# Kernel optimization log

Measured on AMD Instinct MI355X. Metric: run time of the kernel, lower is better.

The kernel has to match this reference:

```python
import jax, jax.numpy as jnp
import numpy as np

B, N, I, K = 2, 8192, 3, 10
LEN_IN = 3 * (K + 1) + 3 * K + I  # 69


def setup_inputs() -> dict:
    key = jax.random.key(0)
    ks = jax.random.split(key, 9)
    return {
        "position": jax.random.normal(ks[0], (B, N, 3), dtype=jnp.float32),
        "velocity": jax.random.normal(ks[1], (B, N, 3), dtype=jnp.float32),
        "init_config": jax.random.normal(ks[2], (B, I), dtype=jnp.float32),
        "W1": jax.random.normal(ks[3], (LEN_IN, 32), dtype=jnp.float32) * 0.1,
        "b1": jnp.zeros((32,), dtype=jnp.float32),
        "W2": jax.random.normal(ks[4], (32, 16), dtype=jnp.float32) * 0.1,
        "b2": jnp.zeros((16,), dtype=jnp.float32),
        "W3": jax.random.normal(ks[5], (16, 6), dtype=jnp.float32) * 0.1,
        "b3": jnp.zeros((6,), dtype=jnp.float32),
    }


def reference(position, velocity, init_config, W1, b1, W2, b2, W3, b3):
    b, n, _ = position.shape
    k = K
    # Squared Euclidean distances (same k-NN ordering as torch.cdist).
    sq = jnp.sum(position * position, axis=-1)  # [B,N]
    d2 = sq[:, :, None] + sq[:, None, :] - 2.0 * jnp.einsum(
        "bnd,bmd->bnm", position, position
    )  # [B,N,N]
    # k+1 nearest (self included), sorted ascending by distance.
    _, idx = jax.lax.top_k(-d2, k + 1)  # [B,N,k+1]
    # Gather neighbor velocities (incl. self) and positions (excl. self).
    vel_nn = jnp.take_along_axis(
        velocity[:, None, :, :], idx[..., None], axis=2
    )  # [B,N,k+1,3]
    pos_nn = jnp.take_along_axis(
        position[:, None, :, :], idx[:, :, 1:, None], axis=2
    )  # [B,N,k,3]
    offset = pos_nn - position[:, :, None, :]  # [B,N,k,3]
    feats = jnp.concatenate(
        [
            vel_nn.reshape(b, n, 3 * (k + 1)),
            offset.reshape(b, n, 3 * k),
            jnp.broadcast_to(init_config[:, None, :], (b, n, init_config.shape[-1])),
        ],
        axis=-1,
    )  # [B,N,6k+3+I]
    h = feats @ W1 + b1
    h = h @ W2 + b2
    pred = h @ W3 + b3  # [B,N,6]
    pred = jnp.concatenate([pred[..., :3] + position, pred[..., 3:]], axis=-1)
    return pred
```

## Files before the change

### kernel.cpp

```cpp
#include <hip/hip_runtime.h>

#define NPTS   8192
#define KNN    11
#define QPB    64
#define NTHR   512
#define NSLICE 8
#define SLEN   (NPTS / NSLICE)
#define DEPTH  12
#define TRIG   9

__global__ __launch_bounds__(NTHR) void knn_mlp(
    const float* __restrict__ pos,
    const float* __restrict__ vel,
    const float* __restrict__ initc,
    const float* __restrict__ W1,
    const float* __restrict__ b1,
    const float* __restrict__ W2,
    const float* __restrict__ b2,
    const float* __restrict__ W3,
    const float* __restrict__ b3,
    float* __restrict__ out) {

    __shared__ __align__(16) float tile[NPTS * 3];
    __shared__ __align__(16) unsigned long long region[NTHR * DEPTH];
    __shared__ float sW[405];

    const int tid  = threadIdx.x;
    const int lane = tid & 63;
    const int wave = tid >> 6;
    const int b    = blockIdx.x >> 7;
    const int n0   = (blockIdx.x & 127) * QPB;
    const int q    = n0 + lane;

    const float* posb = pos + b * NPTS * 3;
    const float* velb = vel + b * NPTS * 3;

    {
        const float4* g4 = (const float4*)posb;
        float4* t4 = (float4*)tile;
#pragma unroll
        for (int i = 0; i < (NPTS * 3 / 4) / NTHR; ++i)
            t4[i * NTHR + tid] = g4[i * NTHR + tid];
    }

    float* sW12 = (float*)region;
    for (int e = tid; e < 66 * 16; e += NTHR) {
        int r = e >> 4, c = e & 15;
        float s = 0.f;
        for (int j = 0; j < 32; ++j) s += W1[r * 32 + j] * W2[j * 16 + c];
        sW12[e] = s;
    }
    if (tid < 16) {
        float s = b2[tid];
        for (int j = 0; j < 32; ++j) s += b1[j] * W2[j * 16 + tid];
        sW12[66 * 16 + tid] = s;
    }
    if (tid < 3) sW[402 + tid] = initc[b * 3 + tid];
    __syncthreads();
    for (int e = tid; e < 66 * 6; e += NTHR) {
        int r = e / 6, c = e - r * 6;
        float s = 0.f;
        for (int j = 0; j < 16; ++j) s += sW12[r * 16 + j] * W3[j * 6 + c];
        sW[e] = s;
    }
    if (tid < 6) {
        float s = b3[tid];
        for (int j = 0; j < 16; ++j) s += sW12[66 * 16 + j] * W3[j * 6 + tid];
        sW[396 + tid] = s;
    }
    __syncthreads();

    const float qx = tile[q * 3 + 0];
    const float qy = tile[q * 3 + 1];
    const float qz = tile[q * 3 + 2];
    const float sqq = __fmaf_rn(qz, qz, __fmaf_rn(qy, qy, __fmul_rn(qx, qx)));

    float d[KNN]; int id[KNN];
#pragma unroll
    for (int m = 0; m < KNN; ++m) { d[m] = 3.0e38f; id[m] = 0x7FFFFFFF; }

    float thr = 3.0e38f;
    int cnt = 0;
    unsigned long long* mybuf = region + tid * DEPTH;

    auto flush = [&]() {
#pragma unroll 1
        for (int k = 0; k < DEPTH; ++k) {
            if (k < cnt) {
                unsigned long long e = mybuf[k];
                float nd = __uint_as_float((unsigned)(e >> 32));
                int   nj = (int)(unsigned)(e & 0xFFFFFFFFull);
                if (nd < d[KNN - 1]) {
                    bool c = true;
#pragma unroll
                    for (int s = KNN - 1; s >= 1; --s) {
                        bool cp = nd < d[s - 1];
                        d[s]  = cp ? d[s - 1] : (c ? nd : d[s]);
                        id[s] = cp ? id[s - 1] : (c ? nj : id[s]);
                        c = cp;
                    }
                    if (c) { d[0] = nd; id[0] = nj; }
                }
            }
        }
        cnt = 0;
        thr = d[KNN - 1];
    };

    auto proc = [&](float cx, float cy, float cz, int j) {
        float sqc = __fmaf_rn(cz, cz, __fmaf_rn(cy, cy, __fmul_rn(cx, cx)));
        float dot = __fmaf_rn(qz, cz, __fmaf_rn(qy, cy, __fmul_rn(qx, cx)));
        float d2  = __fmaf_rn(-2.0f, dot, __fadd_rn(sqq, sqc));
        if (d2 < thr) {
            mybuf[cnt] = (((unsigned long long)__float_as_uint(d2)) << 32)
                         | (unsigned)j;
            ++cnt;
        }
    };

    const int base = wave * SLEN;
    for (int m = 0; m < SLEN; m += 4) {
        int j = base + m;
        const float4* cp = (const float4*)&tile[j * 3];
        float4 A = cp[0], B = cp[1], C = cp[2];
        proc(A.x, A.y, A.z, j + 0);
        proc(A.w, B.x, B.y, j + 1);
        proc(B.z, B.w, C.x, j + 2);
        proc(C.y, C.z, C.w, j + 3);
        if (__any(cnt >= TRIG)) flush();
    }
    flush();

    __syncthreads();
    float* pd = (float*)region;
    int*   pi = (int*)(pd + NTHR * KNN);
#pragma unroll
    for (int m = 0; m < KNN; ++m) { pd[tid * KNN + m] = d[m]; pi[tid * KNN + m] = id[m]; }
    __syncthreads();

    if (tid < QPB) {
        int p[NSLICE]; float hd[NSLICE]; int hi[NSLICE];
#pragma unroll
        for (int s = 0; s < NSLICE; ++s) {
            p[s]  = 0;
            hd[s] = pd[(s * 64 + tid) * KNN];
            hi[s] = pi[(s * 64 + tid) * KNN];
        }
        float acc[6];
#pragma unroll
        for (int c = 0; c < 6; ++c) acc[c] = sW[396 + c];

        for (int r = 0; r < KNN; ++r) {
            float bd = 3.9e38f; int bi = 0x7FFFFFFF; int bs = 0;
#pragma unroll
            for (int s = 0; s < NSLICE; ++s) {
                bool better = (hd[s] < bd) || (hd[s] == bd && hi[s] < bi);
                bs = better ? s : bs;
                bi = better ? hi[s] : bi;
                bd = better ? hd[s] : bd;
            }
            {
                int pp = ++p[bs];
                if (pp < KNN) {
                    hd[bs] = pd[(bs * 64 + tid) * KNN + pp];
                    hi[bs] = pi[(bs * 64 + tid) * KNN + pp];
                } else { hd[bs] = 3.9e38f; hi[bs] = 0x7FFFFFFF; }
            }

            int bg = ((unsigned)bi < (unsigned)NPTS) ? bi : 0;

            const float* vp = velb + bg * 3;
            float vx = vp[0], vy = vp[1], vz = vp[2];
            const float* w = &sW[r * 18];
#pragma unroll
            for (int c = 0; c < 6; ++c) {
                acc[c] += vx * w[c];
                acc[c] += vy * w[6 + c];
                acc[c] += vz * w[12 + c];
            }
            if (r >= 1) {
                float ox = tile[bg * 3 + 0] - qx;
                float oy = tile[bg * 3 + 1] - qy;
                float oz = tile[bg * 3 + 2] - qz;
                const float* w2 = &sW[(33 + (r - 1) * 3) * 6];
#pragma unroll
                for (int c = 0; c < 6; ++c) {
                    acc[c] += ox * w2[c];
                    acc[c] += oy * w2[6 + c];
                    acc[c] += oz * w2[12 + c];
                }
            }
        }
#pragma unroll
        for (int k3 = 0; k3 < 3; ++k3) {
            const float* w3 = &sW[(63 + k3) * 6];
            float iv = sW[402 + k3];
#pragma unroll
            for (int c = 0; c < 6; ++c) acc[c] += iv * w3[c];
        }
        acc[0] += qx; acc[1] += qy; acc[2] += qz;

        float* op = out + (b * NPTS + q) * 6;
#pragma unroll
        for (int c = 0; c < 6; ++c) op[c] = acc[c];
    }
}

extern "C" void kernel_launch(void* const* d_in, const int* in_sizes, int n_in,
                              void* d_out, int out_size, void* d_ws, size_t ws_size,
                              hipStream_t stream) {
    (void)in_sizes; (void)n_in; (void)out_size; (void)d_ws; (void)ws_size;
    const float* pos   = (const float*)d_in[0];
    const float* vel   = (const float*)d_in[1];
    const float* initc = (const float*)d_in[2];
    const float* W1    = (const float*)d_in[3];
    const float* b1    = (const float*)d_in[4];
    const float* W2    = (const float*)d_in[5];
    const float* b2    = (const float*)d_in[6];
    const float* W3    = (const float*)d_in[7];
    const float* b3    = (const float*)d_in[8];
    float* out = (float*)d_out;

    knn_mlp<<<256, NTHR, 0, stream>>>(pos, vel, initc, W1, b1, W2, b2, W3, b3, out);
}
```

Baseline: 192.2 us.

## Stream candidate positions from global memory and cache only squared norms in LDS

New measurement: 194.6 us. Within noise of the previous version (+1.3%).

```diff
diff --git a/kernel.cpp b/kernel.cpp
--- a/kernel.cpp
+++ b/kernel.cpp
@@ -21,7 +21,7 @@
     const float* __restrict__ b3,
     float* __restrict__ out) {
 
-    __shared__ __align__(16) float tile[NPTS * 3];
+    __shared__ __align__(16) float ssq[NPTS];
     __shared__ __align__(16) unsigned long long region[NTHR * DEPTH];
     __shared__ float sW[405];
 
@@ -35,14 +35,12 @@
     const float* posb = pos + b * NPTS * 3;
     const float* velb = vel + b * NPTS * 3;
 
-    {
-        const float4* g4 = (const float4*)posb;
-        float4* t4 = (float4*)tile;
-#pragma unroll
-        for (int i = 0; i < (NPTS * 3 / 4) / NTHR; ++i)
-            t4[i * NTHR + tid] = g4[i * NTHR + tid];
-    }
-
+    for (int a = tid; a < NPTS; a += NTHR) {
+        float x = posb[a * 3 + 0];
+        float y = posb[a * 3 + 1];
+        float z = posb[a * 3 + 2];
+        ssq[a] = __fmaf_rn(z, z, __fmaf_rn(y, y, __fmul_rn(x, x)));
+    }
     float* sW12 = (float*)region;
     for (int e = tid; e < 66 * 16; e += NTHR) {
         int r = e >> 4, c = e & 15;
@@ -70,10 +68,10 @@
     }
     __syncthreads();
 
-    const float qx = tile[q * 3 + 0];
-    const float qy = tile[q * 3 + 1];
-    const float qz = tile[q * 3 + 2];
-    const float sqq = __fmaf_rn(qz, qz, __fmaf_rn(qy, qy, __fmul_rn(qx, qx)));
+    const float qx = posb[q * 3 + 0];
+    const float qy = posb[q * 3 + 1];
+    const float qz = posb[q * 3 + 2];
+    const float sqq = ssq[q];
 
     float d[KNN]; int id[KNN];
 #pragma unroll
@@ -81,13 +79,12 @@
 
     float thr = 3.0e38f;
     int cnt = 0;
-    unsigned long long* mybuf = region + tid * DEPTH;
 
     auto flush = [&]() {
 #pragma unroll 1
-        for (int k = 0; k < DEPTH; ++k) {
+        for (int k = 0; __any(k < cnt); ++k) {
             if (k < cnt) {
-                unsigned long long e = mybuf[k];
+                unsigned long long e = region[k * NTHR + tid];
                 float nd = __uint_as_float((unsigned)(e >> 32));
                 int   nj = (int)(unsigned)(e & 0xFFFFFFFFull);
                 if (nd < d[KNN - 1]) {
@@ -107,27 +104,33 @@
         thr = d[KNN - 1];
     };
 
-    auto proc = [&](float cx, float cy, float cz, int j) {
-        float sqc = __fmaf_rn(cz, cz, __fmaf_rn(cy, cy, __fmul_rn(cx, cx)));
+    auto proc = [&](float cx, float cy, float cz, float sqc, int j) {
         float dot = __fmaf_rn(qz, cz, __fmaf_rn(qy, cy, __fmul_rn(qx, cx)));
         float d2  = __fmaf_rn(-2.0f, dot, __fadd_rn(sqq, sqc));
         if (d2 < thr) {
-            mybuf[cnt] = (((unsigned long long)__float_as_uint(d2)) << 32)
-                         | (unsigned)j;
+            region[cnt * NTHR + tid] =
+                (((unsigned long long)__float_as_uint(d2)) << 32) | (unsigned)j;
             ++cnt;
         }
     };
 
     const int base = wave * SLEN;
+    const float4* gp = (const float4*)(posb + base * 3);
+    const float4* sp = (const float4*)(ssq + base);
+    float4 A = gp[0], Bv = gp[1], C = gp[2];
+    float4 S = sp[0];
     for (int m = 0; m < SLEN; m += 4) {
+        int mn = (m + 4 < SLEN) ? (m + 4) : 0;
+        int fi = (mn >> 2) * 3;
+        float4 nA = gp[fi], nB = gp[fi + 1], nC = gp[fi + 2];
+        float4 nS = sp[mn >> 2];
         int j = base + m;
-        const float4* cp = (const float4*)&tile[j * 3];
-        float4 A = cp[0], B = cp[1], C = cp[2];
-        proc(A.x, A.y, A.z, j + 0);
-        proc(A.w, B.x, B.y, j + 1);
-        proc(B.z, B.w, C.x, j + 2);
-        proc(C.y, C.z, C.w, j + 3);
+        proc(A.x,  A.y,  A.z,  S.x, j + 0);
+        proc(A.w,  Bv.x, Bv.y, S.y, j + 1);
+        proc(Bv.z, Bv.w, C.x,  S.z, j + 2);
+        proc(C.y,  C.z,  C.w,  S.w, j + 3);
         if (__any(cnt >= TRIG)) flush();
+        A = nA; Bv = nB; C = nC; S = nS;
     }
     flush();
 
@@ -179,9 +182,9 @@
                 acc[c] += vz * w[12 + c];
             }
             if (r >= 1) {
-                float ox = tile[bg * 3 + 0] - qx;
-                float oy = tile[bg * 3 + 1] - qy;
-                float oz = tile[bg * 3 + 2] - qz;
+                float ox = posb[bg * 3 + 0] - qx;
+                float oy = posb[bg * 3 + 1] - qy;
+                float oz = posb[bg * 3 + 2] - qz;
                 const float* w2 = &sW[(33 + (r - 1) * 3) * 6];
 #pragma unroll
                 for (int c = 0; c < 6; ++c) {
```
